# Performance work log

Measured on AMD Instinct MI355X. Metric: run time of the kernel, lower is better.

## Reference

```python
import jax, jax.numpy as jnp
import numpy as np

B, L, WORD, H = 16, 32, 512, 1024
HALF = H // 2
TEMP = 1.0


def setup_inputs() -> dict:
    key = jax.random.key(0)
    ks = jax.random.split(key, 12)
    sd = 0.05
    f32 = jnp.float32
    # torch LSTMCell combined bias with forget-gate bias = 1 (gate order i,f,g,o)
    b_lstm = jnp.concatenate([jnp.zeros(HALF), jnp.ones(HALF), jnp.zeros(2 * HALF)]).astype(f32)
    return {
        "sentence_embedding": jax.random.normal(ks[0], (B, L, WORD), f32),
        "length": jax.random.randint(ks[1], (B,), L // 2, L + 1),
        "W_ih_f": jax.random.normal(ks[2], (4 * HALF, WORD), f32) * sd,
        "W_hh_f": jax.random.normal(ks[3], (4 * HALF, HALF), f32) * sd,
        "b_f": b_lstm,
        "W_ih_b": jax.random.normal(ks[4], (4 * HALF, WORD), f32) * sd,
        "W_hh_b": jax.random.normal(ks[5], (4 * HALF, HALF), f32) * sd,
        "b_b": b_lstm,
        "W_rank1": jax.random.normal(ks[6], (256, WORD + 1), f32) * sd,
        "W_rank2": jax.random.normal(ks[7], (1, 256), f32) * sd,
        "W_comp": jax.random.normal(ks[8], (5 * H, 3 * H), f32) * 0.02,
        "b_comp": jnp.zeros((5 * H,), f32),
    }


def _lstm(xs, W_ih, W_hh, b):
    # xs: (L, B, D) -> hs, cs: (B, L, HALF); torch LSTMCell gate order i,f,g,o
    n = xs.shape[1]
    hdim = W_hh.shape[1]

    def step(carry, xt):
        h, c = carry
        g = xt @ W_ih.T + h @ W_hh.T + b
        i, f, gg, o = jnp.split(g, 4, axis=1)
        c = jax.nn.sigmoid(f) * c + jax.nn.sigmoid(i) * jnp.tanh(gg)
        h = jax.nn.sigmoid(o) * jnp.tanh(c)
        return (h, c), (h, c)

    init = (jnp.zeros((n, hdim), xs.dtype), jnp.zeros((n, hdim), xs.dtype))
    _, (hs, cs) = jax.lax.scan(step, init, xs)
    return hs.transpose(1, 0, 2), cs.transpose(1, 0, 2)


def _rev_padded(x, lengths):
    # reverse the first lengths[b] timesteps of each sequence, keep padding in place
    t = np.arange(x.shape[1])
    idx = np.where(t[None, :] < lengths[:, None], lengths[:, None] - 1 - t[None, :], t[None, :])
    return jnp.take_along_axis(x, jnp.asarray(idx)[:, :, None], axis=1)


def _rank_score(seg, W1, W2):
    l = seg.shape[0]
    pos = (2.0 * jnp.arange(l, dtype=seg.dtype) / l - 1.0)[:, None]
    xy = jnp.concatenate([seg, pos], axis=1)
    return jax.nn.relu(xy @ W1.T) @ W2.T  # (l, 1)


def _compose(lst, rst, xst, Wc, bc):
    # Nary tree-LSTM composition over (left, right, current) states; None -> zeros
    hx, cx = xst
    zero = jnp.zeros_like(hx)
    hl, cl = lst if lst is not None else (zero, zero)
    hr, cr = rst if rst is not None else (zero, zero)
    g = jnp.concatenate([hl, hr, hx], axis=1) @ Wc.T + bc  # (1, 5H)
    i, fl, fr, u, o = jnp.split(g, 5, axis=1)
    c = jax.nn.sigmoid(fl) * cl + jax.nn.sigmoid(fr) * cr + jax.nn.sigmoid(i) * jnp.tanh(u)
    h = jax.nn.sigmoid(o) * jnp.tanh(c)
    return h, c


def _build(emb, hs, cs, start, end, W1, W2, Wc, bc, sent, splits, record):
    if end == start:
        return None
    if end == start + 1:
        return (hs[start:start + 1], cs[start:start + 1])
    logits_t = _rank_score(emb[start:end], W1, W2).T  # (1, l)
    y_soft = jax.nn.softmax(logits_t / TEMP, axis=1)
    if record:
        k = int(jnp.argmax(y_soft[0]))
        splits[(sent, start, end)] = k
    else:
        k = splits[(sent, start, end)]
    hard = jnp.zeros_like(y_soft).at[0, k].set(1.0)
    gate = jax.lax.stop_gradient(hard - y_soft) + y_soft  # straight-through estimator
    h = gate @ hs[start:end]
    c = gate @ cs[start:end]
    pos = start + k
    left = _build(emb, hs, cs, start, pos, W1, W2, Wc, bc, sent, splits, record)
    right = _build(emb, hs, cs, pos + 1, end, W1, W2, Wc, bc, sent, splits, record)
    return _compose(left, right, (h, c), Wc, bc)


def _forward(sentence_embedding, length, W_ih_f, W_hh_f, b_f, W_ih_b, W_hh_b, b_b,
             W_rank1, W_rank2, W_comp, b_comp, splits, record):
    lengths = np.asarray(length)
    hs_f, cs_f = _lstm(sentence_embedding.transpose(1, 0, 2), W_ih_f, W_hh_f, b_f)
    x_bw = _rev_padded(sentence_embedding, lengths)
    hs_b, cs_b = _lstm(x_bw.transpose(1, 0, 2), W_ih_b, W_hh_b, b_b)
    hs_b = _rev_padded(hs_b, lengths)
    cs_b = _rev_padded(cs_b, lengths)
    hs = jnp.concatenate([hs_f, hs_b], axis=2)  # (B, L, H)
    cs = jnp.concatenate([cs_f, cs_b], axis=2)
    h_out, c_out = [], []
    for i in range(sentence_embedding.shape[0]):
        st = _build(sentence_embedding[i], hs[i], cs[i], 0, int(lengths[i]),
                    W_rank1, W_rank2, W_comp, b_comp, i, splits, record)
        h_out.append(st[0])
        c_out.append(st[1])
    return jnp.concatenate(h_out, axis=0), jnp.concatenate(c_out, axis=0)


def reference(sentence_embedding, length, W_ih_f, W_hh_f, b_f, W_ih_b, W_hh_b, b_b,
              W_rank1, W_rank2, W_comp, b_comp):
    return _forward(sentence_embedding, length, W_ih_f, W_hh_f, b_f,
                    W_ih_b, W_hh_b, b_b, W_rank1, W_rank2, W_comp, b_comp, {}, True)
```

## Files before the change

### kernel.cpp

```cpp
#include <hip/hip_runtime.h>
#include <math.h>

#define NB 16
#define SL 32
#define H5 5120
#define K3 3072

typedef __attribute__((ext_vector_type(8))) short short8;
typedef __attribute__((ext_vector_type(4))) float floatx4;
typedef __attribute__((ext_vector_type(4))) int intx4;

__device__ __forceinline__ float sigf(float x) { return 1.0f / (1.0f + expf(-x)); }

__device__ __forceinline__ unsigned short f2bf(float x) {
  union { float f; unsigned int u; } v;
  v.f = x;
  unsigned int r = v.u + 0x7FFFu + ((v.u >> 16) & 1u);
  return (unsigned short)(r >> 16);
}

__device__ __forceinline__ void bar32(int* flags, int idx, int mygen) {
  asm volatile("s_waitcnt vmcnt(0)" ::: "memory");
  __syncthreads();
  const int tid = threadIdx.x;
  if (tid == 0)
    __hip_atomic_store(&flags[idx], mygen, __ATOMIC_RELAXED,
                       __HIP_MEMORY_SCOPE_AGENT);
  if (tid < 64) {
    const int off = (tid & 7) * 4;
    int ok;
    do {
      intx4 f;
      asm volatile("global_load_dwordx4 %0, %1, off sc0 sc1\n\t"
                   "s_waitcnt vmcnt(0)"
                   : "=&v"(f) : "v"(flags + off) : "memory");
      ok = (f.x >= mygen) & (f.y >= mygen) & (f.z >= mygen) & (f.w >= mygen);
    } while (__all(ok) == 0);
  }
  __syncthreads();
}

__device__ __forceinline__ void bar_rounds(int* flags, int* gen, int bid, int mygen) {
  asm volatile("s_waitcnt vmcnt(0)" ::: "memory");
  __syncthreads();
  const int tid = threadIdx.x;
  if (tid < 64) {
    if (tid == 0)
      __hip_atomic_store(&flags[bid], mygen, __ATOMIC_RELAXED,
                         __HIP_MEMORY_SCOPE_AGENT);
    if (bid == 0) {
      int ok;
      do {
        intx4 f0, f1;
        asm volatile("global_load_dwordx4 %0, %2, off sc0 sc1\n\t"
                     "global_load_dwordx4 %1, %3, off sc0 sc1\n\t"
                     "s_waitcnt vmcnt(0)"
                     : "=&v"(f0), "=&v"(f1)
                     : "v"(flags + tid * 8), "v"(flags + tid * 8 + 4)
                     : "memory");
        ok = (f0.x >= mygen) & (f0.y >= mygen) & (f0.z >= mygen) & (f0.w >= mygen)
           & (f1.x >= mygen) & (f1.y >= mygen) & (f1.z >= mygen) & (f1.w >= mygen);
      } while (__all(ok) == 0);
      if (tid == 0)
        __hip_atomic_store(gen, mygen, __ATOMIC_RELAXED,
                           __HIP_MEMORY_SCOPE_AGENT);
    } else if (tid == 0) {
      while (__hip_atomic_load(gen, __ATOMIC_RELAXED,
                               __HIP_MEMORY_SCOPE_AGENT) < mygen)
        __builtin_amdgcn_s_sleep(2);
    }
  }
  __syncthreads();
}


__global__ void k_zero3(float* a, int na, float* b, int nb_, float* c, int nc) {
  const int stride = gridDim.x * blockDim.x;
  int i = blockIdx.x * blockDim.x + threadIdx.x;
  for (int k = i; k < na; k += stride) a[k] = 0.0f;
  for (int k = i; k < nb_; k += stride) b[k] = 0.0f;
  for (int k = i; k < nc; k += stride) c[k] = 0.0f;
}

__global__ void k_conv5(const float* s0, unsigned short* d0, int n0,
                        const float* s1, unsigned short* d1, int n1,
                        const float* s2, unsigned short* d2, int n2,
                        const float* s3, unsigned short* d3, int n3,
                        const float* s4, unsigned short* d4, int n4)
{
  const float* s; unsigned short* d; int n;
  switch (blockIdx.y) {
    case 0: s = s0; d = d0; n = n0; break;
    case 1: s = s1; d = d1; n = n1; break;
    case 2: s = s2; d = d2; n = n2; break;
    case 3: s = s3; d = d3; n = n3; break;
    default: s = s4; d = d4; n = n4; break;
  }
  const int nf4 = n >> 2;
  for (int i = blockIdx.x * blockDim.x + threadIdx.x; i < nf4; i += gridDim.x * blockDim.x) {
    const float4 v = *(const float4*)&s[i * 4];
    ushort4 o;
    o.x = f2bf(v.x); o.y = f2bf(v.y); o.z = f2bf(v.z); o.w = f2bf(v.w);
    *(ushort4*)&d[i * 4] = o;
  }
}

__device__ void gemm_body(const float* __restrict__ A, const float* __restrict__ W,
                          float* __restrict__ out, int bx, int by)
{
  __shared__ __align__(16) float sm[2 * 16 * 68];
  float* As = sm;
  float* Ws = sm + 16 * 68;
  const int tid = threadIdx.x;
  const int tx = tid & 15, ty = tid >> 4;
  const int g0 = bx * 64, r0 = by * 64;
  float acc[4][4];
#pragma unroll
  for (int i = 0; i < 4; ++i)
#pragma unroll
    for (int j = 0; j < 4; ++j) acc[i][j] = 0.0f;
  const int ks = tid & 15, rr = tid >> 4;
  for (int kt = 0; kt < 512; kt += 16) {
#pragma unroll
    for (int rep = 0; rep < 4; ++rep) {
      As[ks * 68 + rep * 16 + rr] = A[(size_t)(r0 + rep * 16 + rr) * 512 + kt + ks];
      Ws[ks * 68 + rep * 16 + rr] = W[(size_t)(g0 + rep * 16 + rr) * 513 + kt + ks];
    }
    __syncthreads();
#pragma unroll
    for (int k = 0; k < 16; ++k) {
      const float4 a4 = *(const float4*)&As[k * 68 + ty * 4];
      const float4 w4 = *(const float4*)&Ws[k * 68 + tx * 4];
      const float av[4] = {a4.x, a4.y, a4.z, a4.w};
      const float wv[4] = {w4.x, w4.y, w4.z, w4.w};
#pragma unroll
      for (int i = 0; i < 4; ++i)
#pragma unroll
        for (int j = 0; j < 4; ++j) acc[i][j] += av[i] * wv[j];
    }
    __syncthreads();
  }
#pragma unroll
  for (int i = 0; i < 4; ++i) {
    const int r = r0 + ty * 4 + i;
    float4 o;
    o.x = acc[i][0]; o.y = acc[i][1]; o.z = acc[i][2]; o.w = acc[i][3];
    *(float4*)&out[(size_t)r * 256 + g0 + tx * 4] = o;
  }
}

__device__ void xproj_body(const unsigned short* __restrict__ embB,
                           const unsigned short* __restrict__ B,
                           float* __restrict__ out, int bx, int by)
{
  __shared__ __align__(16) unsigned short As[128 * 40];
  __shared__ __align__(16) unsigned short Bs[128 * 40];
  const int tid = threadIdx.x;
  const int g0 = bx * 128;
  const int r0 = by * 128;
  const int wave = tid >> 6, lane = tid & 63;
  const int wm = wave >> 1, wn = wave & 1;
  const int l15 = lane & 15, quad = lane >> 4;
  floatx4 acc[4][4];
#pragma unroll
  for (int mt = 0; mt < 4; ++mt)
#pragma unroll
    for (int nt = 0; nt < 4; ++nt) acc[mt][nt] = (floatx4){0.f, 0.f, 0.f, 0.f};
  for (int kt = 0; kt < 512; kt += 32) {
    __syncthreads();
#pragma unroll
    for (int p = 0; p < 2; ++p) {
      const int i = tid + p * 256;
      const int row = i >> 2, q = i & 3;
      *(uint4*)&As[row * 40 + q * 8] = *(const uint4*)&embB[(size_t)(r0 + row) * 512 + kt + q * 8];
      *(uint4*)&Bs[row * 40 + q * 8] = *(const uint4*)&B[(size_t)(g0 + row) * 512 + kt + q * 8];
    }
    __syncthreads();
    short8 af[4], bfr[4];
#pragma unroll
    for (int mt = 0; mt < 4; ++mt)
      af[mt] = *(const short8*)&As[(wm * 64 + mt * 16 + l15) * 40 + quad * 8];
#pragma unroll
    for (int nt = 0; nt < 4; ++nt)
      bfr[nt] = *(const short8*)&Bs[(wn * 64 + nt * 16 + l15) * 40 + quad * 8];
#pragma unroll
    for (int mt = 0; mt < 4; ++mt)
#pragma unroll
      for (int nt = 0; nt < 4; ++nt)
        acc[mt][nt] = __builtin_amdgcn_mfma_f32_16x16x32_bf16(af[mt], bfr[nt], acc[mt][nt], 0, 0, 0);
  }
#pragma unroll
  for (int nt = 0; nt < 4; ++nt) {
    const int col = g0 + wn * 64 + nt * 16 + l15;
#pragma unroll
    for (int mt = 0; mt < 4; ++mt)
#pragma unroll
      for (int i = 0; i < 4; ++i) {
        const int row = r0 + wm * 64 + mt * 16 + quad * 4 + i;
        out[(size_t)row * 2048 + col] = acc[mt][nt][i];
      }
  }
}

__global__ __launch_bounds__(256)
void k_proj(const float* __restrict__ emb, const float* __restrict__ Wr1,
            float* __restrict__ E1,
            const unsigned short* __restrict__ embB,
            const unsigned short* __restrict__ WfB,
            const unsigned short* __restrict__ WbB,
            float* __restrict__ Xf, float* __restrict__ Xb)
{
  const int bid = blockIdx.x;
  if (bid < 32) {
    gemm_body(emb, Wr1, E1, bid & 3, bid >> 2);
  } else {
    const int idx = bid - 32;
    const int bz = idx >> 6, rem = idx & 63;
    xproj_body(embB, bz ? WbB : WfB, bz ? Xb : Xf, rem & 15, rem >> 4);
  }
}

__global__ __launch_bounds__(256)
void k_mfma_gemm(const unsigned short* __restrict__ U, const unsigned short* __restrict__ WcB,
                 const float* __restrict__ bc, float* __restrict__ gB)
{
  __shared__ __align__(16) unsigned short As[128 * 40];
  __shared__ __align__(16) unsigned short Bs[64 * 40];
  const int bid = blockIdx.x;
  const int r0 = (bid / 80) * 128;
  const int g0 = (bid % 80) * 64;
  const int tid = threadIdx.x;
  const int wave = tid >> 6, lane = tid & 63;
  const int wm = wave >> 1, wn = wave & 1;
  const int l15 = lane & 15, quad = lane >> 4;
  floatx4 acc[4][2];
#pragma unroll
  for (int mf = 0; mf < 4; ++mf)
#pragma unroll
    for (int nt = 0; nt < 2; ++nt) acc[mf][nt] = (floatx4){0.f, 0.f, 0.f, 0.f};
  const int a_row = tid >> 2, a_q = tid & 3;
  for (int kt = 0; kt < K3; kt += 32) {
    __syncthreads();
#pragma unroll
    for (int p = 0; p < 2; ++p) {
      const int i = tid + p * 256;
      const int row = i >> 2, q = i & 3;
      *(uint4*)&As[row * 40 + q * 8] = *(const uint4*)&U[(size_t)(r0 + row) * K3 + kt + q * 8];
    }
    *(uint4*)&Bs[a_row * 40 + a_q * 8] = *(const uint4*)&WcB[(size_t)(g0 + a_row) * K3 + kt + a_q * 8];
    __syncthreads();
    short8 af[4], bfr[2];
#pragma unroll
    for (int mf = 0; mf < 4; ++mf)
      af[mf] = *(const short8*)&As[(wm * 64 + mf * 16 + l15) * 40 + quad * 8];
#pragma unroll
    for (int nt = 0; nt < 2; ++nt)
      bfr[nt] = *(const short8*)&Bs[(wn * 32 + nt * 16 + l15) * 40 + quad * 8];
#pragma unroll
    for (int mf = 0; mf < 4; ++mf)
#pragma unroll
      for (int nt = 0; nt < 2; ++nt)
        acc[mf][nt] = __builtin_amdgcn_mfma_f32_16x16x32_bf16(af[mf], bfr[nt], acc[mf][nt], 0, 0, 0);
  }
#pragma unroll
  for (int nt = 0; nt < 2; ++nt) {
    const int col = g0 + wn * 32 + nt * 16 + l15;
    const float bias = bc[col];
#pragma unroll
    for (int mf = 0; mf < 4; ++mf)
#pragma unroll
      for (int i = 0; i < 4; ++i) {
        const int row = r0 + wm * 64 + mf * 16 + quad * 4 + i;
        gB[(size_t)row * H5 + col] = acc[mf][nt][i] + bias;
      }
  }
}

__device__ void scan_body(const float* __restrict__ Xf, const float* __restrict__ Xb,
                          const unsigned short* __restrict__ WhfB,
                          const unsigned short* __restrict__ WhbB,
                          const float* __restrict__ bf, const float* __restrict__ bb,
                          const int* __restrict__ len,
                          unsigned short* __restrict__ hbB, float* __restrict__ cbuf,
                          float* __restrict__ hs, float* __restrict__ cs,
                          int* __restrict__ bar, int bid)
{
  const int dir = bid >> 5;
  const int hjt = bid & 31;
  const int tid = threadIdx.x;
  const int wave = tid >> 6, lane = tid & 63;
  const int l15 = lane & 15, quad = lane >> 4;
  const unsigned short* Wh = dir ? WhbB : WhfB;
  const float* bias = dir ? bb : bf;
  const float* X = dir ? Xb : Xf;
  int* myflags = &bar[528 + dir * 32];
  __shared__ float sg[4 * 16 * 17];
  const int jg = wave * 512 + hjt * 16 + l15;
  short8 wfr[16];
#pragma unroll
  for (int k8 = 0; k8 < 16; ++k8)
    wfr[k8] = *(const short8*)&Wh[(size_t)jg * 512 + k8 * 32 + quad * 8];
  const int bb_ = tid >> 4, j = tid & 15;
  const int hj = hjt * 16 + j;
  const int Lb = len[bb_];
  const float bi_i = bias[hj];
  const float bi_f = bias[512 + hj];
  const float bi_g = bias[1024 + hj];
  const float bi_o = bias[1536 + hj];
  for (int t = 0; t < SL; ++t) {
    const int pp = t & 1;
    const unsigned short* hp = hbB + (size_t)(dir * 2 + pp) * 8192;
    unsigned short* hn = hbB + (size_t)(dir * 2 + (pp ^ 1)) * 8192;
    const float* cp = cbuf + (size_t)(dir * 2 + pp) * 8192;
    float* cn = cbuf + (size_t)(dir * 2 + (pp ^ 1)) * 8192;
    int xidx = t;
    if (dir) xidx = (t < Lb) ? (Lb - 1 - t) : t;
    const float* xr = X + (size_t)(bb_ * SL + xidx) * 2048;
    const float x0 = xr[hj];
    const float x1 = xr[512 + hj];
    const float x2 = xr[1024 + hj];
    const float x3 = xr[1536 + hj];
    const float cprev = cp[bb_ * 512 + hj];
    short8 afr[16];
#pragma unroll
    for (int k8 = 0; k8 < 16; ++k8)
      asm volatile("global_load_dwordx4 %0, %1, off sc0 sc1"
                   : "=&v"(afr[k8])
                   : "v"(&hp[(size_t)l15 * 512 + k8 * 32 + quad * 8]));
    asm volatile("s_waitcnt vmcnt(0)" ::: "memory");
    __builtin_amdgcn_sched_barrier(0);
    floatx4 acc = (floatx4){0.f, 0.f, 0.f, 0.f};
#pragma unroll
    for (int k8 = 0; k8 < 16; ++k8)
      acc = __builtin_amdgcn_mfma_f32_16x16x32_bf16(afr[k8], wfr[k8], acc, 0, 0, 0);
#pragma unroll
    for (int i = 0; i < 4; ++i)
      sg[wave * 272 + (quad * 4 + i) * 17 + l15] = acc[i];
    __syncthreads();
    const float gi = sg[0 * 272 + bb_ * 17 + j] + x0 + bi_i;
    const float gf = sg[1 * 272 + bb_ * 17 + j] + x1 + bi_f;
    const float gg = sg[2 * 272 + bb_ * 17 + j] + x2 + bi_g;
    const float go = sg[3 * 272 + bb_ * 17 + j] + x3 + bi_o;
    const float cnew = sigf(gf) * cprev + sigf(gi) * tanhf(gg);
    const float hnew = sigf(go) * tanhf(cnew);
    cn[bb_ * 512 + hj] = cnew;
    const unsigned int hb16 = f2bf(hnew);
    asm volatile("global_store_short %0, %1, off sc0 sc1"
                 :: "v"(&hn[bb_ * 512 + hj]), "v"(hb16) : "memory");
    const int pos = dir ? xidx : t;
    const int col = dir ? (512 + hj) : hj;
    hs[(size_t)(bb_ * SL + pos) * 1024 + col] = hnew;
    cs[(size_t)(bb_ * SL + pos) * 1024 + col] = cnew;
    if (t != SL - 1) bar32(myflags, hjt, t + 1);
  }
}

__device__ void score_body(const float* __restrict__ E1, const float* __restrict__ Wr1,
                           const float* __restrict__ Wr2, const int* __restrict__ len,
                           int* __restrict__ ksplit, int* __restrict__ sflag,
                           int b, int s)
{
  const int tid = threadIdx.x;
  const int L = len[b];
  if (s + 2 <= L) {
    __shared__ float e[32 * 257];
    __shared__ float w1p[256];
    __shared__ float w2s[256];
    __shared__ float red[32 * 8];
    __shared__ float sc[32];
    const int nrow = 32 - s;
    for (int i = tid; i < nrow * 256; i += 256) {
      const int rr = i >> 8, q = i & 255;
      e[rr * 257 + q] = E1[(size_t)(b * SL + s + rr) * 256 + q];
    }
    w1p[tid] = Wr1[tid * 513 + 512];
    w2s[tid] = Wr2[tid];
    __syncthreads();
    const int t_ = tid & 31, jg = tid >> 5;
    const int lmax = L - s;
    for (int l = 2; l <= lmax; ++l) {
      float part = 0.0f;
      if (t_ < l) {
        const float pos = 2.0f * (float)t_ / (float)l - 1.0f;
        const float* er = e + t_ * 257;
        for (int q = jg * 32; q < jg * 32 + 32; ++q) {
          const float v = er[q] + pos * w1p[q];
          part += fmaxf(v, 0.0f) * w2s[q];
        }
      }
      red[t_ * 8 + jg] = part;
      __syncthreads();
      if (jg == 0 && t_ < l) {
        float su = 0.0f;
        for (int q = 0; q < 8; ++q) su += red[t_ * 8 + q];
        sc[t_] = su;
      }
      __syncthreads();
      if (tid == 0) {
        int k = 0;
        float best = sc[0];
        for (int q = 1; q < l; ++q)
          if (sc[q] > best) { best = sc[q]; k = q; }
        __hip_atomic_store(&ksplit[(b * 32 + s) * 33 + l], k,
                           __ATOMIC_RELAXED, __HIP_MEMORY_SCOPE_AGENT);
      }
      __syncthreads();
    }
  }
  __syncthreads();
  if (tid == 0) {
    asm volatile("s_waitcnt vmcnt(0)" ::: "memory");
    __hip_atomic_store(&sflag[b * 31 + s], 1,
                       __ATOMIC_RELAXED, __HIP_MEMORY_SCOPE_AGENT);
  }
}

__device__ void walk_body(const int* __restrict__ ksplit, const int* __restrict__ len,
                          int* __restrict__ meta, int* __restrict__ sflag, int b)
{
  const int tid = threadIdx.x;
  if (tid < 64) {
    int ok;
    do {
      int v = 1;
      if (tid < 31)
        v = __hip_atomic_load(&sflag[b * 31 + tid], __ATOMIC_RELAXED,
                              __HIP_MEMORY_SCOPE_AGENT);
      ok = (v != 0);
    } while (__all(ok) == 0);
  }
  __syncthreads();
  __shared__ int ks[32 * 33];
  __shared__ int stk[96];
  for (int i = tid; i < 32 * 33; i += 256)
    ks[i] = __hip_atomic_load(&ksplit[b * 1056 + i], __ATOMIC_RELAXED,
                              __HIP_MEMORY_SCOPE_AGENT);
  __syncthreads();
  if (tid != 0) return;
  int* own = meta;
  int* lt = meta + 512;
  int* li = meta + 1024;
  int* rt = meta + 1536;
  int* ri = meta + 2048;
  int* dep = meta + 2560;
  int* nn = meta + 3072;
  int* dcnt = meta + 3088;
  int* lcnt = meta + 3120;
  int* dlist = meta + 3152;
  int* llist = meta + 19536;
  int sp = 0, nn_ = 1;
  stk[0] = 0; stk[1] = len[b]; stk[2] = 0;
  sp = 1;
  while (sp > 0) {
    sp--;
    const int s = stk[sp * 3], eN = stk[sp * 3 + 1], nid = stk[sp * 3 + 2];
    const int l = eN - s;
    const int k = ks[s * 33 + l];
    const int m = b * 32 + nid;
    own[m] = s + k;
    if (k == 0) { lt[m] = 0; li[m] = 0; }
    else if (k == 1) { lt[m] = 1; li[m] = s; }
    else {
      const int id = nn_++;
      lt[m] = 2; li[m] = id;
      stk[sp * 3] = s; stk[sp * 3 + 1] = s + k; stk[sp * 3 + 2] = id; sp++;
    }
    const int rl = l - k - 1;
    if (rl == 0) { rt[m] = 0; ri[m] = 0; }
    else if (rl == 1) { rt[m] = 1; ri[m] = s + k + 1; }
    else {
      const int id = nn_++;
      rt[m] = 2; ri[m] = id;
      stk[sp * 3] = s + k + 1; stk[sp * 3 + 1] = eN; stk[sp * 3 + 2] = id; sp++;
    }
  }
  nn[b] = nn_;
  for (int i = nn_ - 1; i >= 0; --i) {
    const int m = b * 32 + i;
    int d = 1;
    if (lt[m] == 2) d = max(d, dep[b * 32 + li[m]] + 1);
    if (rt[m] == 2) d = max(d, dep[b * 32 + ri[m]] + 1);
    dep[m] = d;
  }
  for (int i = 0; i < nn_; ++i) {
    const int m = b * 32 + i;
    const int r = dep[m];
    const int idx = atomicAdd(&dcnt[r], 1);
    dlist[r * 512 + idx] = m;
    if (lt[m] == 2 || rt[m] == 2) {
      const int lx = atomicAdd(&lcnt[r], 1);
      llist[r * 512 + lx] = m;
    }
  }
}

__global__ __launch_bounds__(256)
void k_scansc(const float* Xf, const float* Xb,
              const unsigned short* WhfB, const unsigned short* WhbB,
              const float* bf, const float* bb, const int* len,
              unsigned short* hbB, float* cbuf, float* hs, float* cs, int* bar,
              const float* E1, const float* Wr1, const float* Wr2, int* ksplit,
              const float* Wc, unsigned short* WcB, int* sflag, int* meta)
{
  const int bid = blockIdx.x;
  if (bid < 64) {
    scan_body(Xf, Xb, WhfB, WhbB, bf, bb, len, hbB, cbuf, hs, cs, bar, bid);
  } else if (bid < 560) {
    const int idx = bid - 64;
    score_body(E1, Wr1, Wr2, len, ksplit, sflag, idx / 31, idx % 31);
  } else if (bid < 688) {
    const int idx = bid - 560;
    const int nf4 = 15728640 >> 2;
    for (int i = idx * 256 + threadIdx.x; i < nf4; i += 128 * 256) {
      const float4 v = *(const float4*)&Wc[i * 4];
      ushort4 o;
      o.x = f2bf(v.x); o.y = f2bf(v.y); o.z = f2bf(v.z); o.w = f2bf(v.w);
      *(ushort4*)&WcB[i * 4] = o;
    }
  } else {
    walk_body(ksplit, len, meta, sflag, bid - 688);
  }
}

__global__ __launch_bounds__(256)
void k_ubuild(const float* __restrict__ hs, const int* __restrict__ meta,
              unsigned short* __restrict__ U)
{
  const int id = blockIdx.x, b = blockIdx.y;
  const int tid = threadIdx.x;
  const int* own = meta;
  const int* lt = meta + 512;
  const int* li = meta + 1024;
  const int* rt = meta + 1536;
  const int* ri = meta + 2048;
  const int* nn = meta + 3072;
  const int m = b * 32 + id;
  unsigned short* u = U + (size_t)m * K3;
  if (id >= nn[b]) {
    for (int i = tid; i < K3; i += 256) u[i] = 0;
    return;
  }
  const float* hl = (lt[m] == 1) ? hs + (size_t)(b * 32 + li[m]) * 1024 : nullptr;
  const float* hr = (rt[m] == 1) ? hs + (size_t)(b * 32 + ri[m]) * 1024 : nullptr;
  const float* hx = hs + (size_t)(b * 32 + own[m]) * 1024;
  for (int i = tid; i < 1024; i += 256) {
    u[i] = hl ? f2bf(hl[i]) : 0;
    u[1024 + i] = hr ? f2bf(hr[i]) : 0;
    u[2048 + i] = f2bf(hx[i]);
  }
}

__global__ __launch_bounds__(256, 2)
void k_rounds(const unsigned short* __restrict__ WcB, const int* __restrict__ meta,
              unsigned short* __restrict__ nodehb,
              const float* __restrict__ gB, const float* __restrict__ cs,
              float* __restrict__ nodec,
              float* __restrict__ out, int* __restrict__ bar,
              const unsigned short* __restrict__ zpad)
{
  const int* lt = meta + 512;
  const int* li = meta + 1024;
  const int* rt = meta + 1536;
  const int* ri = meta + 2048;
  const int* dcnt = meta + 3088;
  const int* dlist = meta + 3152;
  __shared__ float scratch[4][16][17];
  __shared__ float gates[16][17];
  const int tid = threadIdx.x;
  const int bid = blockIdx.x;
  const int wave = tid >> 6, lane = tid & 63;
  const int l15 = lane & 15, quad = lane >> 4;
  const int j0 = bid * 2;
  const int cc = (l15 < 10) ? l15 : l15 - 10;
  const size_t wrow = (size_t)((cc >> 1) * 1024 + j0 + (cc & 1)) * K3;
  const int kbase = wave * 256 + quad * 8;
  short8 wreg[16];
#pragma unroll
  for (int i = 0; i < 8; ++i) {
    wreg[i]     = *(const short8*)&WcB[wrow + kbase + i * 32];
    wreg[8 + i] = *(const short8*)&WcB[wrow + 1024 + kbase + i * 32];
  }
  const int rnd = tid >> 4, rc = tid & 15;
  int bgen = 0;
  for (int r = 1; r <= 31; ++r) {
    const int cnt = dcnt[r];
    if (cnt == 0) break;
    if (r >= 2) { ++bgen; bar_rounds(bar, &bar[512], bid, bgen); }
    for (int c0 = 0; c0 < cnt; c0 += 16) {
      float gBv = 0.0f;
      if (rc < 10 && c0 + rnd < cnt) {
        const int nodeP = dlist[r * 512 + c0 + rnd];
        gBv = gB[(size_t)nodeP * H5 + (rc >> 1) * 1024 + j0 + (rc & 1)];
      }
      const int ma = c0 + l15;
      const unsigned short* pl = zpad;
      const unsigned short* pr = zpad;
      if (ma < cnt) {
        const int node = dlist[r * 512 + ma];
        const int base = node & ~31;
        if (lt[node] == 2) pl = nodehb + (size_t)(base + li[node]) * 1024;
        if (rt[node] == 2) pr = nodehb + (size_t)(base + ri[node]) * 1024;
      }
      short8 al[8], ar[8];
#pragma unroll
      for (int i = 0; i < 8; ++i)
        asm volatile("global_load_dwordx4 %0, %1, off sc0 sc1"
                     : "=&v"(al[i]) : "v"(pl + kbase + i * 32));
#pragma unroll
      for (int i = 0; i < 8; ++i)
        asm volatile("global_load_dwordx4 %0, %1, off sc0 sc1"
                     : "=&v"(ar[i]) : "v"(pr + kbase + i * 32));
      floatx4 acc = (floatx4){0.f, 0.f, 0.f, 0.f};
      asm volatile("s_waitcnt vmcnt(8)" ::: "memory");
      __builtin_amdgcn_sched_barrier(0);
#pragma unroll
      for (int ks = 0; ks < 8; ++ks)
        acc = __builtin_amdgcn_mfma_f32_16x16x32_bf16(al[ks], wreg[ks], acc, 0, 0, 0);
      asm volatile("s_waitcnt vmcnt(0)" ::: "memory");
      __builtin_amdgcn_sched_barrier(0);
#pragma unroll
      for (int ks = 0; ks < 8; ++ks)
        acc = __builtin_amdgcn_mfma_f32_16x16x32_bf16(ar[ks], wreg[8 + ks], acc, 0, 0, 0);
      __syncthreads();
#pragma unroll
      for (int i = 0; i < 4; ++i)
        scratch[wave][quad * 4 + i][l15] = acc[i];
      __syncthreads();
      if (rc < 10)
        gates[rnd][rc] = gBv + scratch[0][rnd][rc] + scratch[1][rnd][rc]
                             + scratch[2][rnd][rc] + scratch[3][rnd][rc];
      __syncthreads();
      if (tid < 16) {
        const int mc = c0 + tid;
        if (mc < cnt) {
          const int node = dlist[r * 512 + mc];
          const int base = node & ~31;
          const int ltv = lt[node], rtv = rt[node];
          const float* clp = (ltv == 2) ? &nodec[(size_t)(base + li[node]) * 1024]
                           : (ltv == 1) ? &cs[(size_t)(base + li[node]) * 1024] : nullptr;
          const float* crp = (rtv == 2) ? &nodec[(size_t)(base + ri[node]) * 1024]
                           : (rtv == 1) ? &cs[(size_t)(base + ri[node]) * 1024] : nullptr;
          unsigned int pk = 0;
#pragma unroll
          for (int jj = 0; jj < 2; ++jj) {
            const int j = j0 + jj;
            const float gi  = gates[tid][0 + jj];
            const float gfl = gates[tid][2 + jj];
            const float gfr = gates[tid][4 + jj];
            const float gu  = gates[tid][6 + jj];
            const float go  = gates[tid][8 + jj];
            const float cl = clp ? clp[j] : 0.0f;
            const float cr = crp ? crp[j] : 0.0f;
            const float c_ = sigf(gfl) * cl + sigf(gfr) * cr + sigf(gi) * tanhf(gu);
            const float h  = sigf(go) * tanhf(c_);
            nodec[(size_t)node * 1024 + j] = c_;
            pk |= ((unsigned int)f2bf(h)) << (16 * jj);
            if ((node & 31) == 0) {
              const int b = node >> 5;
              out[b * 1024 + j] = h;
              out[16384 + b * 1024 + j] = c_;
            }
          }
          asm volatile("global_store_dword %0, %1, off sc0 sc1"
                       :: "v"(nodehb + (size_t)node * 1024 + j0), "v"(pk)
                       : "memory");
        }
      }
    }
  }
}

extern "C" void kernel_launch(void* const* d_in, const int* in_sizes, int n_in,
                              void* d_out, int out_size, void* d_ws, size_t ws_size,
                              hipStream_t stream) {
  const float* emb = (const float*)d_in[0];
  const int* len = (const int*)d_in[1];
  const float* Wihf = (const float*)d_in[2];
  const float* Whhf = (const float*)d_in[3];
  const float* bf = (const float*)d_in[4];
  const float* Wihb = (const float*)d_in[5];
  const float* Whhb = (const float*)d_in[6];
  const float* bb = (const float*)d_in[7];
  const float* Wr1 = (const float*)d_in[8];
  const float* Wr2 = (const float*)d_in[9];
  const float* Wc = (const float*)d_in[10];
  const float* bc = (const float*)d_in[11];
  float* out = (float*)d_out;

  float* ws = (float*)d_ws;
  float* Xf = ws;
  float* Xb = Xf + 1048576;
  float* hs = Xb + 1048576;
  float* cs = hs + 524288;
  float* E1 = cs + 524288;
  unsigned short* U = (unsigned short*)(E1 + 131072);
  float* gB = (float*)U + 786432;
  float* nodeh = gB + 2621440;
  float* nodec = nodeh + 524288;
  unsigned short* nodehb = (unsigned short*)(nodec + 524288);
  float* cbuf = (float*)nodehb + 262144;
  unsigned short* hbB = (unsigned short*)(cbuf + 32768);
  unsigned short* WcB = (unsigned short*)((float*)hbB + 16384);
  unsigned short* WihfB = WcB + 15728640;
  unsigned short* WihbB = WihfB + 1048576;
  unsigned short* WhhfB = WihbB + 1048576;
  unsigned short* WhhbB = WhhfB + 1048576;
  unsigned short* embB = WhhbB + 1048576;
  int* meta = (int*)(embB + 262144);
  int* ksplit = meta + 36096;
  int* bar = ksplit + 16896;
  unsigned short* zpad = (unsigned short*)(bar + 1024);
  int* sflag = bar + 1536;

  k_zero3<<<128, 256, 0, stream>>>(cbuf, 49152, (float*)(meta + 3088), 64,
                                   (float*)bar, 2048);
  k_conv5<<<dim3(512, 5), 256, 0, stream>>>(
      emb, embB, 262144, Wihf, WihfB, 1048576, Wihb, WihbB, 1048576,
      Whhf, WhhfB, 1048576, Whhb, WhhbB, 1048576);
  k_proj<<<160, 256, 0, stream>>>(emb, Wr1, E1, embB, WihfB, WihbB, Xf, Xb);
  k_scansc<<<704, 256, 0, stream>>>(Xf, Xb, WhhfB, WhhbB, bf, bb, len, hbB,
                                    cbuf, hs, cs, bar, E1, Wr1, Wr2, ksplit,
                                    Wc, WcB, sflag, meta);
  k_ubuild<<<dim3(32, 16), 256, 0, stream>>>(hs, meta, U);
  k_mfma_gemm<<<320, 256, 0, stream>>>(U, WcB, bc, gB);
  k_rounds<<<512, 256, 0, stream>>>(WcB, meta, nodehb, gB, cs,
                                    nodec, out, bar, zpad);
}
```

Measured before the change: 510.1 us.

## Fuse bf16 conversions and zeroing into consumer kernels, drop ubuild and conv passes

Removes the separate zeroing, fp32-to-bf16 conversion, and U-matrix build kernels. The conversions now happen inside the projection GEMM, the scan weight load, and the compose GEMM A-tile load, which gathers hs rows through per-row pointers held in shared memory. The zeroing moves into extra blocks of the projection kernel. This cuts three launches and the intermediate bf16 buffers, but every GEMM tile now repeats the conversion work and reads twice as many fp32 bytes.

```diff
diff --git a/kernel.cpp b/kernel.cpp
--- a/kernel.cpp
+++ b/kernel.cpp
@@ -74,37 +74,6 @@
 }
 
 
-__global__ void k_zero3(float* a, int na, float* b, int nb_, float* c, int nc) {
-  const int stride = gridDim.x * blockDim.x;
-  int i = blockIdx.x * blockDim.x + threadIdx.x;
-  for (int k = i; k < na; k += stride) a[k] = 0.0f;
-  for (int k = i; k < nb_; k += stride) b[k] = 0.0f;
-  for (int k = i; k < nc; k += stride) c[k] = 0.0f;
-}
-
-__global__ void k_conv5(const float* s0, unsigned short* d0, int n0,
-                        const float* s1, unsigned short* d1, int n1,
-                        const float* s2, unsigned short* d2, int n2,
-                        const float* s3, unsigned short* d3, int n3,
-                        const float* s4, unsigned short* d4, int n4)
-{
-  const float* s; unsigned short* d; int n;
-  switch (blockIdx.y) {
-    case 0: s = s0; d = d0; n = n0; break;
-    case 1: s = s1; d = d1; n = n1; break;
-    case 2: s = s2; d = d2; n = n2; break;
-    case 3: s = s3; d = d3; n = n3; break;
-    default: s = s4; d = d4; n = n4; break;
-  }
-  const int nf4 = n >> 2;
-  for (int i = blockIdx.x * blockDim.x + threadIdx.x; i < nf4; i += gridDim.x * blockDim.x) {
-    const float4 v = *(const float4*)&s[i * 4];
-    ushort4 o;
-    o.x = f2bf(v.x); o.y = f2bf(v.y); o.z = f2bf(v.z); o.w = f2bf(v.w);
-    *(ushort4*)&d[i * 4] = o;
-  }
-}
-
 __device__ void gemm_body(const float* __restrict__ A, const float* __restrict__ W,
                           float* __restrict__ out, int bx, int by)
 {
@@ -149,8 +118,8 @@
   }
 }
 
-__device__ void xproj_body(const unsigned short* __restrict__ embB,
-                           const unsigned short* __restrict__ B,
+__device__ void xproj_body(const float* __restrict__ emb,
+                           const float* __restrict__ W,
                            float* __restrict__ out, int bx, int by)
 {
   __shared__ __align__(16) unsigned short As[128 * 40];
@@ -172,8 +141,21 @@
     for (int p = 0; p < 2; ++p) {
       const int i = tid + p * 256;
       const int row = i >> 2, q = i & 3;
-      *(uint4*)&As[row * 40 + q * 8] = *(const uint4*)&embB[(size_t)(r0 + row) * 512 + kt + q * 8];
-      *(uint4*)&Bs[row * 40 + q * 8] = *(const uint4*)&B[(size_t)(g0 + row) * 512 + kt + q * 8];
+      const float* pe = &emb[(size_t)(r0 + row) * 512 + kt + q * 8];
+      const float* pw = &W[(size_t)(g0 + row) * 512 + kt + q * 8];
+      const float4 a0 = *(const float4*)pe;
+      const float4 a1 = *(const float4*)(pe + 4);
+      const float4 b0 = *(const float4*)pw;
+      const float4 b1 = *(const float4*)(pw + 4);
+      ushort4 ua0, ua1, ub0, ub1;
+      ua0.x = f2bf(a0.x); ua0.y = f2bf(a0.y); ua0.z = f2bf(a0.z); ua0.w = f2bf(a0.w);
+      ua1.x = f2bf(a1.x); ua1.y = f2bf(a1.y); ua1.z = f2bf(a1.z); ua1.w = f2bf(a1.w);
+      ub0.x = f2bf(b0.x); ub0.y = f2bf(b0.y); ub0.z = f2bf(b0.z); ub0.w = f2bf(b0.w);
+      ub1.x = f2bf(b1.x); ub1.y = f2bf(b1.y); ub1.z = f2bf(b1.z); ub1.w = f2bf(b1.w);
+      *(ushort4*)&As[row * 40 + q * 8] = ua0;
+      *(ushort4*)&As[row * 40 + q * 8 + 4] = ua1;
+      *(ushort4*)&Bs[row * 40 + q * 8] = ub0;
+      *(ushort4*)&Bs[row * 40 + q * 8 + 4] = ub1;
     }
     __syncthreads();
     short8 af[4], bfr[4];
@@ -205,80 +187,29 @@
 __global__ __launch_bounds__(256)
 void k_proj(const float* __restrict__ emb, const float* __restrict__ Wr1,
             float* __restrict__ E1,
-            const unsigned short* __restrict__ embB,
-            const unsigned short* __restrict__ WfB,
-            const unsigned short* __restrict__ WbB,
-            float* __restrict__ Xf, float* __restrict__ Xb)
+            const float* __restrict__ Wihf, const float* __restrict__ Wihb,
+            float* __restrict__ Xf, float* __restrict__ Xb,
+            float* __restrict__ cbuf, float* __restrict__ zm, float* __restrict__ zb)
 {
   const int bid = blockIdx.x;
   if (bid < 32) {
     gemm_body(emb, Wr1, E1, bid & 3, bid >> 2);
-  } else {
+  } else if (bid < 160) {
     const int idx = bid - 32;
     const int bz = idx >> 6, rem = idx & 63;
-    xproj_body(embB, bz ? WbB : WfB, bz ? Xb : Xf, rem & 15, rem >> 4);
-  }
-}
-
-__global__ __launch_bounds__(256)
-void k_mfma_gemm(const unsigned short* __restrict__ U, const unsigned short* __restrict__ WcB,
-                 const float* __restrict__ bc, float* __restrict__ gB)
-{
-  __shared__ __align__(16) unsigned short As[128 * 40];
-  __shared__ __align__(16) unsigned short Bs[64 * 40];
-  const int bid = blockIdx.x;
-  const int r0 = (bid / 80) * 128;
-  const int g0 = (bid % 80) * 64;
-  const int tid = threadIdx.x;
-  const int wave = tid >> 6, lane = tid & 63;
-  const int wm = wave >> 1, wn = wave & 1;
-  const int l15 = lane & 15, quad = lane >> 4;
-  floatx4 acc[4][2];
-#pragma unroll
-  for (int mf = 0; mf < 4; ++mf)
-#pragma unroll
-    for (int nt = 0; nt < 2; ++nt) acc[mf][nt] = (floatx4){0.f, 0.f, 0.f, 0.f};
-  const int a_row = tid >> 2, a_q = tid & 3;
-  for (int kt = 0; kt < K3; kt += 32) {
-    __syncthreads();
-#pragma unroll
-    for (int p = 0; p < 2; ++p) {
-      const int i = tid + p * 256;
-      const int row = i >> 2, q = i & 3;
-      *(uint4*)&As[row * 40 + q * 8] = *(const uint4*)&U[(size_t)(r0 + row) * K3 + kt + q * 8];
-    }
-    *(uint4*)&Bs[a_row * 40 + a_q * 8] = *(const uint4*)&WcB[(size_t)(g0 + a_row) * K3 + kt + a_q * 8];
-    __syncthreads();
-    short8 af[4], bfr[2];
-#pragma unroll
-    for (int mf = 0; mf < 4; ++mf)
-      af[mf] = *(const short8*)&As[(wm * 64 + mf * 16 + l15) * 40 + quad * 8];
-#pragma unroll
-    for (int nt = 0; nt < 2; ++nt)
-      bfr[nt] = *(const short8*)&Bs[(wn * 32 + nt * 16 + l15) * 40 + quad * 8];
-#pragma unroll
-    for (int mf = 0; mf < 4; ++mf)
-#pragma unroll
-      for (int nt = 0; nt < 2; ++nt)
-        acc[mf][nt] = __builtin_amdgcn_mfma_f32_16x16x32_bf16(af[mf], bfr[nt], acc[mf][nt], 0, 0, 0);
-  }
-#pragma unroll
-  for (int nt = 0; nt < 2; ++nt) {
-    const int col = g0 + wn * 32 + nt * 16 + l15;
-    const float bias = bc[col];
-#pragma unroll
-    for (int mf = 0; mf < 4; ++mf)
-#pragma unroll
-      for (int i = 0; i < 4; ++i) {
-        const int row = r0 + wm * 64 + mf * 16 + quad * 4 + i;
-        gB[(size_t)row * H5 + col] = acc[mf][nt][i] + bias;
-      }
+    xproj_body(emb, bz ? Wihb : Wihf, bz ? Xb : Xf, rem & 15, rem >> 4);
+  } else {
+    const int i0 = (bid - 160) * 256 + threadIdx.x;
+    const int stride = 32 * 256;
+    for (int k = i0; k < 49152; k += stride) cbuf[k] = 0.0f;
+    for (int k = i0; k < 64; k += stride) zm[k] = 0.0f;
+    for (int k = i0; k < 2048; k += stride) zb[k] = 0.0f;
   }
 }
 
 __device__ void scan_body(const float* __restrict__ Xf, const float* __restrict__ Xb,
-                          const unsigned short* __restrict__ WhfB,
-                          const unsigned short* __restrict__ WhbB,
+                          const float* __restrict__ Whhf,
+                          const float* __restrict__ Whhb,
                           const float* __restrict__ bf, const float* __restrict__ bb,
                           const int* __restrict__ len,
                           unsigned short* __restrict__ hbB, float* __restrict__ cbuf,
@@ -290,7 +221,7 @@
   const int tid = threadIdx.x;
   const int wave = tid >> 6, lane = tid & 63;
   const int l15 = lane & 15, quad = lane >> 4;
-  const unsigned short* Wh = dir ? WhbB : WhfB;
+  const float* Wh = dir ? Whhb : Whhf;
   const float* bias = dir ? bb : bf;
   const float* X = dir ? Xb : Xf;
   int* myflags = &bar[528 + dir * 32];
@@ -298,8 +229,13 @@
   const int jg = wave * 512 + hjt * 16 + l15;
   short8 wfr[16];
 #pragma unroll
-  for (int k8 = 0; k8 < 16; ++k8)
-    wfr[k8] = *(const short8*)&Wh[(size_t)jg * 512 + k8 * 32 + quad * 8];
+  for (int k8 = 0; k8 < 16; ++k8) {
+    const float* pw = &Wh[(size_t)jg * 512 + k8 * 32 + quad * 8];
+    short8 w;
+#pragma unroll
+    for (int e = 0; e < 8; ++e) w[e] = (short)f2bf(pw[e]);
+    wfr[k8] = w;
+  }
   const int bb_ = tid >> 4, j = tid & 15;
   const int hj = hjt * 16 + j;
   const int Lb = len[bb_];
@@ -496,7 +432,7 @@
 
 __global__ __launch_bounds__(256)
 void k_scansc(const float* Xf, const float* Xb,
-              const unsigned short* WhfB, const unsigned short* WhbB,
+              const float* Whhf, const float* Whhb,
               const float* bf, const float* bb, const int* len,
               unsigned short* hbB, float* cbuf, float* hs, float* cs, int* bar,
               const float* E1, const float* Wr1, const float* Wr2, int* ksplit,
@@ -504,7 +440,7 @@
 {
   const int bid = blockIdx.x;
   if (bid < 64) {
-    scan_body(Xf, Xb, WhfB, WhbB, bf, bb, len, hbB, cbuf, hs, cs, bar, bid);
+    scan_body(Xf, Xb, Whhf, Whhb, bf, bb, len, hbB, cbuf, hs, cs, bar, bid);
   } else if (bid < 560) {
     const int idx = bid - 64;
     score_body(E1, Wr1, Wr2, len, ksplit, sflag, idx / 31, idx % 31);
@@ -523,30 +459,92 @@
 }
 
 __global__ __launch_bounds__(256)
-void k_ubuild(const float* __restrict__ hs, const int* __restrict__ meta,
-              unsigned short* __restrict__ U)
-{
-  const int id = blockIdx.x, b = blockIdx.y;
-  const int tid = threadIdx.x;
-  const int* own = meta;
-  const int* lt = meta + 512;
-  const int* li = meta + 1024;
-  const int* rt = meta + 1536;
-  const int* ri = meta + 2048;
-  const int* nn = meta + 3072;
-  const int m = b * 32 + id;
-  unsigned short* u = U + (size_t)m * K3;
-  if (id >= nn[b]) {
-    for (int i = tid; i < K3; i += 256) u[i] = 0;
-    return;
-  }
-  const float* hl = (lt[m] == 1) ? hs + (size_t)(b * 32 + li[m]) * 1024 : nullptr;
-  const float* hr = (rt[m] == 1) ? hs + (size_t)(b * 32 + ri[m]) * 1024 : nullptr;
-  const float* hx = hs + (size_t)(b * 32 + own[m]) * 1024;
-  for (int i = tid; i < 1024; i += 256) {
-    u[i] = hl ? f2bf(hl[i]) : 0;
-    u[1024 + i] = hr ? f2bf(hr[i]) : 0;
-    u[2048 + i] = f2bf(hx[i]);
+void k_mfma_gemm(const float* __restrict__ hs, const int* __restrict__ meta,
+                 const unsigned short* __restrict__ WcB,
+                 const float* __restrict__ bc, float* __restrict__ gB)
+{
+  __shared__ __align__(16) unsigned short As[128 * 40];
+  __shared__ __align__(16) unsigned short Bs[64 * 40];
+  __shared__ const float* rowsrc[128][3];
+  const int bid = blockIdx.x;
+  const int r0 = (bid / 80) * 128;
+  const int g0 = (bid % 80) * 64;
+  const int tid = threadIdx.x;
+  const int wave = tid >> 6, lane = tid & 63;
+  const int wm = wave >> 1, wn = wave & 1;
+  const int l15 = lane & 15, quad = lane >> 4;
+  if (tid < 128) {
+    const int m = r0 + tid;
+    const int b = m >> 5, id = m & 31;
+    const int* lt = meta + 512;
+    const int* li = meta + 1024;
+    const int* rt = meta + 1536;
+    const int* ri = meta + 2048;
+    const int* own = meta;
+    const int* nn = meta + 3072;
+    const float* p0 = nullptr;
+    const float* p1 = nullptr;
+    const float* p2 = nullptr;
+    if (id < nn[b]) {
+      if (lt[m] == 1) p0 = hs + (size_t)(b * 32 + li[m]) * 1024;
+      if (rt[m] == 1) p1 = hs + (size_t)(b * 32 + ri[m]) * 1024;
+      p2 = hs + (size_t)(b * 32 + own[m]) * 1024;
+    }
+    rowsrc[tid][0] = p0;
+    rowsrc[tid][1] = p1;
+    rowsrc[tid][2] = p2;
+  }
+  floatx4 acc[4][2];
+#pragma unroll
+  for (int mf = 0; mf < 4; ++mf)
+#pragma unroll
+    for (int nt = 0; nt < 2; ++nt) acc[mf][nt] = (floatx4){0.f, 0.f, 0.f, 0.f};
+  const int a_row = tid >> 2, a_q = tid & 3;
+  for (int kt = 0; kt < K3; kt += 32) {
+    __syncthreads();
+#pragma unroll
+    for (int p = 0; p < 2; ++p) {
+      const int i = tid + p * 256;
+      const int row = i >> 2, q = i & 3;
+      const int kk = kt + q * 8;
+      const int seg = kk >> 10, kl = kk & 1023;
+      const float* sp = rowsrc[row][seg];
+      ushort4 u0 = {0, 0, 0, 0}, u1 = {0, 0, 0, 0};
+      if (sp) {
+        const float4 a0 = *(const float4*)(sp + kl);
+        const float4 a1 = *(const float4*)(sp + kl + 4);
+        u0.x = f2bf(a0.x); u0.y = f2bf(a0.y); u0.z = f2bf(a0.z); u0.w = f2bf(a0.w);
+        u1.x = f2bf(a1.x); u1.y = f2bf(a1.y); u1.z = f2bf(a1.z); u1.w = f2bf(a1.w);
+      }
+      *(ushort4*)&As[row * 40 + q * 8] = u0;
+      *(ushort4*)&As[row * 40 + q * 8 + 4] = u1;
+    }
+    *(uint4*)&Bs[a_row * 40 + a_q * 8] = *(const uint4*)&WcB[(size_t)(g0 + a_row) * K3 + kt + a_q * 8];
+    __syncthreads();
+    short8 af[4], bfr[2];
+#pragma unroll
+    for (int mf = 0; mf < 4; ++mf)
+      af[mf] = *(const short8*)&As[(wm * 64 + mf * 16 + l15) * 40 + quad * 8];
+#pragma unroll
+    for (int nt = 0; nt < 2; ++nt)
+      bfr[nt] = *(const short8*)&Bs[(wn * 32 + nt * 16 + l15) * 40 + quad * 8];
+#pragma unroll
+    for (int mf = 0; mf < 4; ++mf)
+#pragma unroll
+      for (int nt = 0; nt < 2; ++nt)
+        acc[mf][nt] = __builtin_amdgcn_mfma_f32_16x16x32_bf16(af[mf], bfr[nt], acc[mf][nt], 0, 0, 0);
+  }
+#pragma unroll
+  for (int nt = 0; nt < 2; ++nt) {
+    const int col = g0 + wn * 32 + nt * 16 + l15;
+    const float bias = bc[col];
+#pragma unroll
+    for (int mf = 0; mf < 4; ++mf)
+#pragma unroll
+      for (int i = 0; i < 4; ++i) {
+        const int row = r0 + wm * 64 + mf * 16 + quad * 4 + i;
+        gB[(size_t)row * H5 + col] = acc[mf][nt][i] + bias;
+      }
   }
 }
 
@@ -701,28 +699,18 @@
   float* cbuf = (float*)nodehb + 262144;
   unsigned short* hbB = (unsigned short*)(cbuf + 32768);
   unsigned short* WcB = (unsigned short*)((float*)hbB + 16384);
-  unsigned short* WihfB = WcB + 15728640;
-  unsigned short* WihbB = WihfB + 1048576;
-  unsigned short* WhhfB = WihbB + 1048576;
-  unsigned short* WhhbB = WhhfB + 1048576;
-  unsigned short* embB = WhhbB + 1048576;
-  int* meta = (int*)(embB + 262144);
+  int* meta = (int*)(WcB + 15728640);
   int* ksplit = meta + 36096;
   int* bar = ksplit + 16896;
   unsigned short* zpad = (unsigned short*)(bar + 1024);
   int* sflag = bar + 1536;
 
-  k_zero3<<<128, 256, 0, stream>>>(cbuf, 49152, (float*)(meta + 3088), 64,
-                                   (float*)bar, 2048);
-  k_conv5<<<dim3(512, 5), 256, 0, stream>>>(
-      emb, embB, 262144, Wihf, WihfB, 1048576, Wihb, WihbB, 1048576,
-      Whhf, WhhfB, 1048576, Whhb, WhhbB, 1048576);
-  k_proj<<<160, 256, 0, stream>>>(emb, Wr1, E1, embB, WihfB, WihbB, Xf, Xb);
-  k_scansc<<<704, 256, 0, stream>>>(Xf, Xb, WhhfB, WhhbB, bf, bb, len, hbB,
+  k_proj<<<192, 256, 0, stream>>>(emb, Wr1, E1, Wihf, Wihb, Xf, Xb,
+                                  cbuf, (float*)(meta + 3088), (float*)bar);
+  k_scansc<<<704, 256, 0, stream>>>(Xf, Xb, Whhf, Whhb, bf, bb, len, hbB,
                                     cbuf, hs, cs, bar, E1, Wr1, Wr2, ksplit,
                                     Wc, WcB, sflag, meta);
-  k_ubuild<<<dim3(32, 16), 256, 0, stream>>>(hs, meta, U);
-  k_mfma_gemm<<<320, 256, 0, stream>>>(U, WcB, bc, gB);
+  k_mfma_gemm<<<320, 256, 0, stream>>>(hs, meta, WcB, bc, gB);
   k_rounds<<<512, 256, 0, stream>>>(WcB, meta, nodehb, gB, cs,
                                     nodec, out, bar, zpad);
 }
```

Result: slower. 562.7 us (+10.3%).
